# Optimization experiments

Hardware: AMD Instinct MI355X
Metric: run time of the kernel (lower is better)

The kernel has to match this reference:

```python
import jax, jax.numpy as jnp
import numpy as np

BEV_H, BEV_W = 50, 50
D_PILLAR = 4
PC = (-51.2, -51.2, -5.0, 51.2, 51.2, 3.0)
S_IMG = 518.0   # input_size; also img H and W used for uv normalization
LN_EPS = 1e-5
FUSE_EPS = 1e-6
C_CTX = 256


def _layernorm(x):
    mu = jnp.mean(x, axis=-1, keepdims=True)
    var = jnp.mean((x - mu) ** 2, axis=-1, keepdims=True)
    return (x - mu) * jax.lax.rsqrt(var + LN_EPS)


def _make_lidar2img(V):
    # realistic surround-view cameras: yaw-rotated extrinsics + pinhole intrinsics
    fx = fy = 400.0
    cx = cy = S_IMG / 2.0
    K = np.array([[fx, 0, cx, 0], [0, fy, cy, 0], [0, 0, 1, 0], [0, 0, 0, 1]], dtype=np.float64)
    mats = []
    for v in range(V):
        th = 2.0 * np.pi * v / V
        f = np.array([np.cos(th), np.sin(th), 0.0])      # camera forward (z)
        l = np.array([-np.sin(th), np.cos(th), 0.0])     # camera x (lateral)
        d = np.array([0.0, 0.0, -1.0])                   # camera y (down)
        R = np.stack([l, d, f], axis=0)
        t = np.array([0.0, 0.0, 1.5])                    # camera position in lidar frame
        E = np.eye(4); E[:3, :3] = R; E[:3, 3] = -R @ t
        mats.append(K @ E)
    return np.stack(mats, axis=0).astype(np.float32)     # (V,4,4)


def setup_inputs() -> dict:
    key = jax.random.key(0)
    k1, = jax.random.split(key, 1)
    B, V, N, C = 1, 6, 37 * 37, 768
    last_tokens = jax.random.normal(k1, (B, V, N, C), dtype=jnp.float32)
    lidar2img = jnp.asarray(_make_lidar2img(V))[None]    # (B,V,4,4)
    return {
        "last_tokens": last_tokens,
        "lidar2img": lidar2img,
        "w_view": jnp.zeros((1, V, 1), dtype=jnp.float32),
        "post_gamma": jnp.ones((C,), dtype=jnp.float32),
        "post_beta": jnp.zeros((C,), dtype=jnp.float32),
        "logits": jnp.zeros((C_CTX, C // C_CTX), dtype=jnp.float32),
        "patch_h": 37,
        "patch_w": 37,
    }


def _projection(lidar2img, dtype):
    # BEVFormer-style 3d reference points -> per-camera uv + visibility mask
    Z = int(round(PC[5] - PC[2]))  # 8
    zs = (jnp.linspace(0.5, Z - 0.5, D_PILLAR, dtype=dtype) / Z)[:, None, None]
    xs = (jnp.linspace(0.5, BEV_W - 0.5, BEV_W, dtype=dtype) / BEV_W)[None, None, :]
    ys = (jnp.linspace(0.5, BEV_H - 0.5, BEV_H, dtype=dtype) / BEV_H)[None, :, None]
    x, y, z = jnp.broadcast_arrays(xs, ys, zs)           # (D,H,W) each
    ref = jnp.stack([x, y, z], axis=-1).reshape(D_PILLAR, BEV_H * BEV_W, 3)
    ref = ref * jnp.array([PC[3] - PC[0], PC[4] - PC[1], PC[5] - PC[2]], dtype) \
        + jnp.array([PC[0], PC[1], PC[2]], dtype)
    ref4 = jnp.concatenate([ref, jnp.ones_like(ref[..., :1])], axis=-1)  # (D,Q,4)
    pts = jnp.einsum('bvij,dqj->bdvqi', lidar2img, ref4)  # (B,D,V,Q,4)
    zc = pts[..., 2]
    valid = zc > 1e-5
    uv = pts[..., :2] / jnp.maximum(zc, 1e-5)[..., None] / S_IMG
    u, v = uv[..., 0], uv[..., 1]
    valid = valid & (u > 0.0) & (u < 1.0) & (v > 0.0) & (v < 1.0)
    # -> (B,V,Q,D)
    tr = lambda a: jnp.transpose(a, (0, 2, 3, 1))
    return tr(u), tr(v), tr(valid)


def reference(last_tokens, lidar2img, w_view, post_gamma, post_beta, logits, patch_h, patch_w):
    B, V, N, C = last_tokens.shape
    Hp, Wp = int(patch_h), int(patch_w)
    Q = BEV_H * BEV_W
    dt = last_tokens.dtype

    # pre-LN over channels (no affine)
    tok = _layernorm(last_tokens)                         # (B,V,N,C)

    u, v, valid = _projection(lidar2img, dt)              # (B,V,Q,D)
    u, v = jax.lax.stop_gradient(u), jax.lax.stop_gradient(v)  # torch: @no_grad

    # pixel coords on the patch grid (align_corners=True grid_sample equivalent)
    x_p = (u * S_IMG + 0.5) / S_IMG * Wp - 0.5
    y_p = (v * S_IMG + 0.5) / S_IMG * Hp - 0.5

    x0 = jnp.floor(x_p); fx = x_p - x0; x0 = x0.astype(jnp.int32)
    y0 = jnp.floor(y_p); fy = y_p - y0; y0 = y0.astype(jnp.int32)

    QD = Q * D_PILLAR
    acc = jnp.zeros((B, V, QD, C), dtype=dt)
    for dx in (0, 1):
        for dy in (0, 1):
            xi, yi = x0 + dx, y0 + dy
            inb = (xi >= 0) & (xi < Wp) & (yi >= 0) & (yi < Hp)  # zeros padding
            w = jnp.where(dx, fx, 1.0 - fx) * jnp.where(dy, fy, 1.0 - fy) * inb.astype(dt)
            idx = jnp.clip(yi, 0, Hp - 1) * Wp + jnp.clip(xi, 0, Wp - 1)
            g = jnp.take_along_axis(tok, idx.reshape(B, V, QD, 1), axis=2)  # (B,V,QD,C)
            acc = acc + w.reshape(B, V, QD, 1) * g
    sampled = acc.reshape(B, V, Q, D_PILLAR, C)

    m = valid.astype(dt)                                  # (B,V,Q,D)
    feat = jnp.einsum('bvqdc,bvqd->bvqc', sampled, m)     # mask-weighted sum over pillar pts
    cnt = jnp.sum(m, axis=-1)                             # (B,V,Q)

    wv = jax.nn.softplus(w_view)                          # (1,V,1) positive per-view weights
    num = jnp.sum(feat * wv[..., None], axis=1)           # (B,Q,C)
    den = jnp.sum(cnt * wv, axis=1)                       # (B,Q)
    fused = num / (den[..., None] + FUSE_EPS)

    h = _layernorm(fused) * post_gamma + post_beta        # post-LN with affine

    g = C // C_CTX
    wg = jax.nn.softmax(logits, axis=-1)                  # (C_CTX, g)
    y = jnp.sum(h.reshape(B, Q, C_CTX, g) * wg[None, None], axis=-1)  # (B,Q,C_CTX)

    return jnp.transpose(y.reshape(B, BEV_H, BEV_W, C_CTX), (0, 3, 1, 2))
```

## Files before the change

### kernel.cpp

```cpp
#include <hip/hip_runtime.h>
#include <math.h>

#define NV      6
#define ND      4
#define NQ      2500
#define NPATCH  1369
#define NROWS   (NV * NPATCH)
#define CTOK    768
#define HP      37
#define WP      37
#define CCTX    256

__device__ __forceinline__ float softplus_f(float x) {
    return (x > 20.0f) ? x : log1pf(expf(x));
}

__global__ __launch_bounds__(256) void ln_stats_kernel(
    const float* __restrict__ tok, float* __restrict__ stats )
{
    const int wave = threadIdx.x >> 6, lane = threadIdx.x & 63;
    const int row = blockIdx.x * 4 + wave;
    if (row >= NROWS) return;
    const float4* x = (const float4*)(tok + (size_t)row * CTOK);
    float s = 0.f, ss = 0.f;
    #pragma unroll
    for (int i = 0; i < 3; ++i) {
        float4 v = x[lane + 64 * i];
        s  += (v.x + v.y) + (v.z + v.w);
        ss += v.x * v.x + v.y * v.y + v.z * v.z + v.w * v.w;
    }
    #pragma unroll
    for (int off = 32; off; off >>= 1) {
        s  += __shfl_down(s,  off, 64);
        ss += __shfl_down(ss, off, 64);
    }
    if (lane == 0) {
        float mu  = s * (1.0f / (float)CTOK);
        float var = ss * (1.0f / (float)CTOK) - mu * mu;
        float rs  = rsqrtf(fmaxf(var, 0.0f) + 1e-5f);
        stats[row * 2 + 0] = mu;
        stats[row * 2 + 1] = rs;
    }
}

__device__ __forceinline__ void block_reduce_2(float& a, float& b, float* sbuf) {
    #pragma unroll
    for (int off = 32; off > 0; off >>= 1) {
        a += __shfl_down(a, off, 64);
        b += __shfl_down(b, off, 64);
    }
    int wave = threadIdx.x >> 6;
    int lane = threadIdx.x & 63;
    if (lane == 0) { sbuf[wave] = a; sbuf[4 + wave] = b; }
    __syncthreads();
    a = sbuf[0] + sbuf[1] + sbuf[2] + sbuf[3];
    b = sbuf[4] + sbuf[5] + sbuf[6] + sbuf[7];
}

__global__ __launch_bounds__(256) void bev_fuse_kernel(
    const float* __restrict__ tok,
    const float* __restrict__ stats,
    const float* __restrict__ lidar2img,
    const float* __restrict__ w_view,
    const float* __restrict__ gamma,
    const float* __restrict__ beta,
    const float* __restrict__ logits,
    float* __restrict__ out)
{
    __shared__ float s_b[NV * ND * 4];
    __shared__ float s_bmu[NV * ND * 4];
    __shared__ int   s_idx[NV * ND * 4];
    __shared__ float s_den[NV * ND];
    __shared__ int   s_cnt;
    __shared__ float sbuf[8];
    __shared__ float s_h[CTOK];

    const int q = blockIdx.x;
    const int t = threadIdx.x;

    if (t == 0) s_cnt = 0;
    __syncthreads();

    if (t < NV * ND) {
        const int v = t >> 2, d = t & 3;
        const int qy = q / 50, qx = q - qy * 50;
        float xf = ((float)qx + 0.5f) * (1.0f / 50.0f);
        float yf = ((float)qy + 0.5f) * (1.0f / 50.0f);
        float zf = (0.5f + (float)d * (7.0f / 3.0f)) * (1.0f / 8.0f);
        float X = xf * 102.4f - 51.2f;
        float Y = yf * 102.4f - 51.2f;
        float Z = zf * 8.0f - 5.0f;
        const float* M = lidar2img + v * 16;
        float px = M[0] * X + M[1] * Y + M[2]  * Z + M[3];
        float py = M[4] * X + M[5] * Y + M[6]  * Z + M[7];
        float pz = M[8] * X + M[9] * Y + M[10] * Z + M[11];
        bool valid = pz > 1e-5f;
        float zc = fmaxf(pz, 1e-5f);
        float uu = px / zc * (1.0f / 518.0f);
        float vv = py / zc * (1.0f / 518.0f);
        valid = valid && (uu > 0.0f) && (uu < 1.0f) && (vv > 0.0f) && (vv < 1.0f);

        float wv = softplus_f(w_view[v]);
        s_den[t] = valid ? wv : 0.0f;

        if (valid) {
            float x_p = (uu * 518.0f + 0.5f) * (37.0f / 518.0f) - 0.5f;
            float y_p = (vv * 518.0f + 0.5f) * (37.0f / 518.0f) - 0.5f;
            float x0f = floorf(x_p), y0f = floorf(y_p);
            float fx = x_p - x0f, fy = y_p - y0f;
            int x0 = (int)x0f, y0 = (int)y0f;
            #pragma unroll
            for (int corner = 0; corner < 4; ++corner) {
                int dx = corner & 1, dy = corner >> 1;
                int xi = x0 + dx, yi = y0 + dy;
                bool inb = (xi >= 0) && (xi < WP) && (yi >= 0) && (yi < HP);
                float w = (dx ? fx : (1.0f - fx)) * (dy ? fy : (1.0f - fy));
                if (inb && w != 0.0f) {
                    int idx = v * NPATCH + yi * WP + xi;
                    float b = w * wv * stats[idx * 2 + 1];
                    int slot = atomicAdd(&s_cnt, 1);
                    s_b[slot]   = b;
                    s_bmu[slot] = b * stats[idx * 2 + 0];
                    s_idx[slot] = idx;
                }
            }
        }
    }
    __syncthreads();

    const int m = s_cnt;

    float den = 0.0f;
    #pragma unroll
    for (int j = 0; j < NV * ND; ++j) den += s_den[j];
    float c0 = 0.0f;
    for (int j = 0; j < m; ++j) c0 += s_bmu[j];

    float f0 = 0.f, f1 = 0.f, f2 = 0.f, f3 = 0.f;
    if (t < 192) {
        const float4* base = (const float4*)tok;
        for (int j = 0; j < m; ++j) {
            float b = s_b[j];
            float4 x = base[(size_t)s_idx[j] * (CTOK / 4) + t];
            f0 = fmaf(b, x.x, f0);
            f1 = fmaf(b, x.y, f1);
            f2 = fmaf(b, x.z, f2);
            f3 = fmaf(b, x.w, f3);
        }
    }
    float inv = 1.0f / (den + 1e-6f);
    f0 = (f0 - c0) * inv;
    f1 = (f1 - c0) * inv;
    f2 = (f2 - c0) * inv;
    f3 = (f3 - c0) * inv;

    float s = 0.f, ss = 0.f;
    if (t < 192) {
        s  = (f0 + f1) + (f2 + f3);
        ss = f0 * f0 + f1 * f1 + f2 * f2 + f3 * f3;
    }
    block_reduce_2(s, ss, sbuf);
    float mu  = s * (1.0f / (float)CTOK);
    float var = ss * (1.0f / (float)CTOK) - mu * mu;
    float rs  = rsqrtf(fmaxf(var, 0.0f) + 1e-5f);

    if (t < 192) {
        int c = t * 4;
        s_h[c + 0] = (f0 - mu) * rs * gamma[c + 0] + beta[c + 0];
        s_h[c + 1] = (f1 - mu) * rs * gamma[c + 1] + beta[c + 1];
        s_h[c + 2] = (f2 - mu) * rs * gamma[c + 2] + beta[c + 2];
        s_h[c + 3] = (f3 - mu) * rs * gamma[c + 3] + beta[c + 3];
    }
    __syncthreads();

    float l0 = logits[t * 3 + 0], l1 = logits[t * 3 + 1], l2 = logits[t * 3 + 2];
    float mx = fmaxf(l0, fmaxf(l1, l2));
    float e0 = expf(l0 - mx), e1 = expf(l1 - mx), e2 = expf(l2 - mx);
    float einv = 1.0f / (e0 + e1 + e2);
    float y = (s_h[t * 3 + 0] * e0 + s_h[t * 3 + 1] * e1 + s_h[t * 3 + 2] * e2) * einv;
    out[(size_t)t * NQ + q] = y;
}

extern "C" void kernel_launch(void* const* d_in, const int* in_sizes, int n_in,
                              void* d_out, int out_size, void* d_ws, size_t ws_size,
                              hipStream_t stream) {
    const float* last_tokens = (const float*)d_in[0];
    const float* lidar2img   = (const float*)d_in[1];
    const float* w_view      = (const float*)d_in[2];
    const float* post_gamma  = (const float*)d_in[3];
    const float* post_beta   = (const float*)d_in[4];
    const float* logits      = (const float*)d_in[5];
    float* out = (float*)d_out;

    float* stats = (float*)d_ws;

    ln_stats_kernel<<<(NROWS + 3) / 4, 256, 0, stream>>>(last_tokens, stats);
    bev_fuse_kernel<<<NQ, 256, 0, stream>>>(last_tokens, stats, lidar2img, w_view,
                                            post_gamma, post_beta, logits, out);
}
```

Baseline: 100.3 us.

## Process four BEV queries per block with one wave per query

Each block now handles four BEV queries, with one 64-lane wave owning each query. Each lane accumulates 12 channels, and the two-sample unrolled gather loop issues more loads in flight. Because a whole query lives in one wave, the LayerNorm reduction uses only wave shuffles and drops the block-level sync and shared buffer. Outputs for the four consecutive queries are staged in shared memory and written as one float4 per context channel, which replaces the scattered scalar stores. The trade-offs are fewer blocks (625), a fixed MAXM of 96 sample slots per query, and q0 alignment that relies on NQ being divisible by 4.

```diff
diff --git a/kernel.cpp b/kernel.cpp
--- a/kernel.cpp
+++ b/kernel.cpp
@@ -10,6 +10,8 @@
 #define HP      37
 #define WP      37
 #define CCTX    256
+#define QT      4
+#define MAXM    96
 
 __device__ __forceinline__ float softplus_f(float x) {
     return (x > 20.0f) ? x : log1pf(expf(x));
@@ -41,20 +43,6 @@
         stats[row * 2 + 0] = mu;
         stats[row * 2 + 1] = rs;
     }
-}
-
-__device__ __forceinline__ void block_reduce_2(float& a, float& b, float* sbuf) {
-    #pragma unroll
-    for (int off = 32; off > 0; off >>= 1) {
-        a += __shfl_down(a, off, 64);
-        b += __shfl_down(b, off, 64);
-    }
-    int wave = threadIdx.x >> 6;
-    int lane = threadIdx.x & 63;
-    if (lane == 0) { sbuf[wave] = a; sbuf[4 + wave] = b; }
-    __syncthreads();
-    a = sbuf[0] + sbuf[1] + sbuf[2] + sbuf[3];
-    b = sbuf[4] + sbuf[5] + sbuf[6] + sbuf[7];
 }
 
 __global__ __launch_bounds__(256) void bev_fuse_kernel(
@@ -67,22 +55,24 @@
     const float* __restrict__ logits,
     float* __restrict__ out)
 {
-    __shared__ float s_b[NV * ND * 4];
-    __shared__ float s_bmu[NV * ND * 4];
-    __shared__ int   s_idx[NV * ND * 4];
-    __shared__ float s_den[NV * ND];
-    __shared__ int   s_cnt;
-    __shared__ float sbuf[8];
-    __shared__ float s_h[CTOK];
-
-    const int q = blockIdx.x;
+    __shared__ float s_b[QT][MAXM];
+    __shared__ float s_bmu[QT][MAXM];
+    __shared__ int   s_idx[QT][MAXM];
+    __shared__ float s_den[QT][NV * ND];
+    __shared__ int   s_cnt[QT];
+    __shared__ float s_y[QT][CCTX];
+
     const int t = threadIdx.x;
-
-    if (t == 0) s_cnt = 0;
+    const int q0 = blockIdx.x * QT;
+
+    if (t < QT) s_cnt[t] = 0;
     __syncthreads();
 
-    if (t < NV * ND) {
-        const int v = t >> 2, d = t & 3;
+    if (t < QT * NV * ND) {
+        const int qi = t / 24;
+        const int p  = t - qi * 24;
+        const int v = p >> 2, d = p & 3;
+        const int q = q0 + qi;
         const int qy = q / 50, qx = q - qy * 50;
         float xf = ((float)qx + 0.5f) * (1.0f / 50.0f);
         float yf = ((float)qy + 0.5f) * (1.0f / 50.0f);
@@ -101,7 +91,7 @@
         valid = valid && (uu > 0.0f) && (uu < 1.0f) && (vv > 0.0f) && (vv < 1.0f);
 
         float wv = softplus_f(w_view[v]);
-        s_den[t] = valid ? wv : 0.0f;
+        s_den[qi][p] = valid ? wv : 0.0f;
 
         if (valid) {
             float x_p = (uu * 518.0f + 0.5f) * (37.0f / 518.0f) - 0.5f;
@@ -118,67 +108,113 @@
                 if (inb && w != 0.0f) {
                     int idx = v * NPATCH + yi * WP + xi;
                     float b = w * wv * stats[idx * 2 + 1];
-                    int slot = atomicAdd(&s_cnt, 1);
-                    s_b[slot]   = b;
-                    s_bmu[slot] = b * stats[idx * 2 + 0];
-                    s_idx[slot] = idx;
+                    int slot = atomicAdd(&s_cnt[qi], 1);
+                    s_b[qi][slot]   = b;
+                    s_bmu[qi][slot] = b * stats[idx * 2 + 0];
+                    s_idx[qi][slot] = idx;
                 }
             }
         }
     }
     __syncthreads();
 
-    const int m = s_cnt;
+    const int w = t >> 6, lane = t & 63;
+    const int m = s_cnt[w];
 
     float den = 0.0f;
     #pragma unroll
-    for (int j = 0; j < NV * ND; ++j) den += s_den[j];
+    for (int p = 0; p < NV * ND; ++p) den += s_den[w][p];
     float c0 = 0.0f;
-    for (int j = 0; j < m; ++j) c0 += s_bmu[j];
-
-    float f0 = 0.f, f1 = 0.f, f2 = 0.f, f3 = 0.f;
-    if (t < 192) {
-        const float4* base = (const float4*)tok;
-        for (int j = 0; j < m; ++j) {
-            float b = s_b[j];
-            float4 x = base[(size_t)s_idx[j] * (CTOK / 4) + t];
-            f0 = fmaf(b, x.x, f0);
-            f1 = fmaf(b, x.y, f1);
-            f2 = fmaf(b, x.z, f2);
-            f3 = fmaf(b, x.w, f3);
-        }
-    }
-    float inv = 1.0f / (den + 1e-6f);
-    f0 = (f0 - c0) * inv;
-    f1 = (f1 - c0) * inv;
-    f2 = (f2 - c0) * inv;
-    f3 = (f3 - c0) * inv;
+    for (int j = 0; j < m; ++j) c0 += s_bmu[w][j];
+
+    const float4* base = (const float4*)tok;
+    const int fp = 3 * lane;
+    float4 a0 = {0,0,0,0}, a1 = {0,0,0,0}, a2 = {0,0,0,0};
+    int j = 0;
+    for (; j + 2 <= m; j += 2) {
+        float b0 = s_b[w][j], b1 = s_b[w][j + 1];
+        const float4* p0 = base + (size_t)s_idx[w][j]     * (CTOK / 4) + fp;
+        const float4* p1 = base + (size_t)s_idx[w][j + 1] * (CTOK / 4) + fp;
+        float4 x0 = p0[0], x1 = p0[1], x2 = p0[2];
+        float4 y0 = p1[0], y1 = p1[1], y2 = p1[2];
+        a0.x = fmaf(b0, x0.x, a0.x); a0.y = fmaf(b0, x0.y, a0.y);
+        a0.z = fmaf(b0, x0.z, a0.z); a0.w = fmaf(b0, x0.w, a0.w);
+        a1.x = fmaf(b0, x1.x, a1.x); a1.y = fmaf(b0, x1.y, a1.y);
+        a1.z = fmaf(b0, x1.z, a1.z); a1.w = fmaf(b0, x1.w, a1.w);
+        a2.x = fmaf(b0, x2.x, a2.x); a2.y = fmaf(b0, x2.y, a2.y);
+        a2.z = fmaf(b0, x2.z, a2.z); a2.w = fmaf(b0, x2.w, a2.w);
+        a0.x = fmaf(b1, y0.x, a0.x); a0.y = fmaf(b1, y0.y, a0.y);
+        a0.z = fmaf(b1, y0.z, a0.z); a0.w = fmaf(b1, y0.w, a0.w);
+        a1.x = fmaf(b1, y1.x, a1.x); a1.y = fmaf(b1, y1.y, a1.y);
+        a1.z = fmaf(b1, y1.z, a1.z); a1.w = fmaf(b1, y1.w, a1.w);
+        a2.x = fmaf(b1, y2.x, a2.x); a2.y = fmaf(b1, y2.y, a2.y);
+        a2.z = fmaf(b1, y2.z, a2.z); a2.w = fmaf(b1, y2.w, a2.w);
+    }
+    if (j < m) {
+        float b0 = s_b[w][j];
+        const float4* p0 = base + (size_t)s_idx[w][j] * (CTOK / 4) + fp;
+        float4 x0 = p0[0], x1 = p0[1], x2 = p0[2];
+        a0.x = fmaf(b0, x0.x, a0.x); a0.y = fmaf(b0, x0.y, a0.y);
+        a0.z = fmaf(b0, x0.z, a0.z); a0.w = fmaf(b0, x0.w, a0.w);
+        a1.x = fmaf(b0, x1.x, a1.x); a1.y = fmaf(b0, x1.y, a1.y);
+        a1.z = fmaf(b0, x1.z, a1.z); a1.w = fmaf(b0, x1.w, a1.w);
+        a2.x = fmaf(b0, x2.x, a2.x); a2.y = fmaf(b0, x2.y, a2.y);
+        a2.z = fmaf(b0, x2.z, a2.z); a2.w = fmaf(b0, x2.w, a2.w);
+    }
+
+    float f[12];
+    {
+        float inv = 1.0f / (den + 1e-6f);
+        f[0]  = (a0.x - c0) * inv; f[1]  = (a0.y - c0) * inv;
+        f[2]  = (a0.z - c0) * inv; f[3]  = (a0.w - c0) * inv;
+        f[4]  = (a1.x - c0) * inv; f[5]  = (a1.y - c0) * inv;
+        f[6]  = (a1.z - c0) * inv; f[7]  = (a1.w - c0) * inv;
+        f[8]  = (a2.x - c0) * inv; f[9]  = (a2.y - c0) * inv;
+        f[10] = (a2.z - c0) * inv; f[11] = (a2.w - c0) * inv;
+    }
 
     float s = 0.f, ss = 0.f;
-    if (t < 192) {
-        s  = (f0 + f1) + (f2 + f3);
-        ss = f0 * f0 + f1 * f1 + f2 * f2 + f3 * f3;
-    }
-    block_reduce_2(s, ss, sbuf);
+    #pragma unroll
+    for (int i = 0; i < 12; ++i) { s += f[i]; ss += f[i] * f[i]; }
+    #pragma unroll
+    for (int off = 32; off; off >>= 1) {
+        s  += __shfl_down(s,  off, 64);
+        ss += __shfl_down(ss, off, 64);
+    }
+    s  = __shfl(s,  0, 64);
+    ss = __shfl(ss, 0, 64);
     float mu  = s * (1.0f / (float)CTOK);
     float var = ss * (1.0f / (float)CTOK) - mu * mu;
     float rs  = rsqrtf(fmaxf(var, 0.0f) + 1e-5f);
 
-    if (t < 192) {
-        int c = t * 4;
-        s_h[c + 0] = (f0 - mu) * rs * gamma[c + 0] + beta[c + 0];
-        s_h[c + 1] = (f1 - mu) * rs * gamma[c + 1] + beta[c + 1];
-        s_h[c + 2] = (f2 - mu) * rs * gamma[c + 2] + beta[c + 2];
-        s_h[c + 3] = (f3 - mu) * rs * gamma[c + 3] + beta[c + 3];
+    const float4* g4 = (const float4*)gamma;
+    const float4* b4 = (const float4*)beta;
+    float4 gv[3] = {g4[fp], g4[fp + 1], g4[fp + 2]};
+    float4 bv[3] = {b4[fp], b4[fp + 1], b4[fp + 2]};
+    const float* gs = (const float*)gv;
+    const float* bs = (const float*)bv;
+    float h[12];
+    #pragma unroll
+    for (int i = 0; i < 12; ++i)
+        h[i] = (f[i] - mu) * rs * gs[i] + bs[i];
+
+    const float4* lg4 = (const float4*)logits;
+    float4 Lv[3] = {lg4[fp], lg4[fp + 1], lg4[fp + 2]};
+    const float* lgv = (const float*)Lv;
+    #pragma unroll
+    for (int jj = 0; jj < 4; ++jj) {
+        float l0 = lgv[jj * 3], l1 = lgv[jj * 3 + 1], l2 = lgv[jj * 3 + 2];
+        float mx = fmaxf(l0, fmaxf(l1, l2));
+        float e0 = expf(l0 - mx), e1 = expf(l1 - mx), e2 = expf(l2 - mx);
+        float einv = 1.0f / (e0 + e1 + e2);
+        s_y[w][lane * 4 + jj] =
+            (h[jj * 3] * e0 + h[jj * 3 + 1] * e1 + h[jj * 3 + 2] * e2) * einv;
     }
     __syncthreads();
 
-    float l0 = logits[t * 3 + 0], l1 = logits[t * 3 + 1], l2 = logits[t * 3 + 2];
-    float mx = fmaxf(l0, fmaxf(l1, l2));
-    float e0 = expf(l0 - mx), e1 = expf(l1 - mx), e2 = expf(l2 - mx);
-    float einv = 1.0f / (e0 + e1 + e2);
-    float y = (s_h[t * 3 + 0] * e0 + s_h[t * 3 + 1] * e1 + s_h[t * 3 + 2] * e2) * einv;
-    out[(size_t)t * NQ + q] = y;
+    float4 o;
+    o.x = s_y[0][t]; o.y = s_y[1][t]; o.z = s_y[2][t]; o.w = s_y[3][t];
+    *(float4*)(out + (size_t)t * NQ + q0) = o;
 }
 
 extern "C" void kernel_launch(void* const* d_in, const int* in_sizes, int n_in,
@@ -195,6 +231,7 @@
     float* stats = (float*)d_ws;
 
     ln_stats_kernel<<<(NROWS + 3) / 4, 256, 0, stream>>>(last_tokens, stats);
-    bev_fuse_kernel<<<NQ, 256, 0, stream>>>(last_tokens, stats, lidar2img, w_view,
-                                            post_gamma, post_beta, logits, out);
-}
+    bev_fuse_kernel<<<NQ / QT, 256, 0, stream>>>(last_tokens, stats, lidar2img,
+                                                 w_view, post_gamma, post_beta,
+                                                 logits, out);
+}
```

After: 98.68 us. No clear change (-1.6%).
